# Kernel tuning notes

Measured on AMD Instinct MI355X. Metric: run time of the kernel, lower is better.

Reference implementation:

```python
import jax, jax.numpy as jnp
import numpy as np

NUM_NODES = 2048
NUM_REL = 8
HIDDEN = 256


def setup_inputs() -> dict:
    key = jax.random.key(0)
    k1, k2, k3 = jax.random.split(key, 3)
    X = jax.random.normal(k1, (NUM_NODES, HIDDEN, NUM_REL), dtype=jnp.float32)
    A = jax.random.uniform(k2, (NUM_NODES, NUM_NODES, NUM_REL), dtype=jnp.float32)
    # nn.init.normal_(std=0.01)
    weight = 0.01 * jax.random.normal(k3, (HIDDEN, HIDDEN, NUM_REL), dtype=jnp.float32)
    return {"X": X, "A": A, "weight": weight}


def _tensor_product(A, B):
    # Faithful to the original: FFT along last (relation) dim, take REAL part of
    # both transformed operands, per-slice matmul, then real part of ifft.
    Af = jnp.real(jnp.fft.fft(A, axis=-1))  # (n1, n2, k)
    Bf = jnp.real(jnp.fft.fft(B, axis=-1))  # (n2, n4, k)
    C = jnp.einsum('nmk,mhk->nhk', Af, Bf)  # batched real matmul over slices k
    return jnp.real(jnp.fft.ifft(C, axis=-1)).astype(A.dtype)


def reference(X, A, weight):
    res = _tensor_product(A, X)          # (num_nodes, hidden, num_rel)
    res = _tensor_product(res, weight)   # (num_nodes, hidden, num_rel)
    return res
```

## Files before the change

kernel.cpp:

```cpp
#include <hip/hip_runtime.h>


typedef __bf16 bf16_t;
typedef __bf16 bf16x2 __attribute__((ext_vector_type(2)));
typedef __bf16 bf16x8 __attribute__((ext_vector_type(8)));
typedef float f32x4 __attribute__((ext_vector_type(4)));

#define R2C 0.70710678118654752f

__device__ __forceinline__ size_t swz(int r, int c, int K) {
  return (size_t)r * K + (c & ~63) + ((((c >> 3) & 7) ^ (r & 7)) << 3) + (c & 7);
}

__device__ __forceinline__ void async_cp16(const void* g, void* l) {
  __builtin_amdgcn_global_load_lds((const __attribute__((address_space(1))) char*)g,
                                   (__attribute__((address_space(3))) char*)l,
                                   16, 0, 0);
}

__device__ __forceinline__ void fwd5(const float x[8], float F[5]) {
  float s04 = x[0] + x[4], d04 = x[0] - x[4];
  float s26 = x[2] + x[6];
  float s15 = x[1] + x[5], s37 = x[3] + x[7];
  float t = (x[1] + x[7]) - (x[3] + x[5]);
  float e = s04 + s26, o = s15 + s37;
  F[0] = e + o;
  F[1] = d04 + R2C * t;
  F[2] = s04 - s26;
  F[3] = d04 - R2C * t;
  F[4] = e - o;
}

__global__ __launch_bounds__(256) void k_pre(const float* __restrict__ X,
                                             const float* __restrict__ A,
                                             const float* __restrict__ W,
                                             bf16_t* __restrict__ Xft,
                                             bf16_t* __restrict__ Af,
                                             bf16_t* __restrict__ Wft) {
  __shared__ bf16_t tx[40][256];
  int b = blockIdx.x;
  if (b < 2048) {
    size_t t = (size_t)b * 256 + threadIdx.x;
    size_t idx = t * 8;
    int n = (int)(idx >> 11), m8 = (int)(idx & 2047);
    const f32x4* p = (const f32x4*)(A + idx * 8);
    float F[8][5];
#pragma unroll
    for (int u = 0; u < 8; u++) {
      f32x4 a = __builtin_nontemporal_load(p + 2 * u);
      f32x4 bb = __builtin_nontemporal_load(p + 2 * u + 1);
      float x[8] = {a.x, a.y, a.z, a.w, bb.x, bb.y, bb.z, bb.w};
      fwd5(x, F[u]);
    }
    size_t pos = (size_t)n * 2048 + (m8 & ~63) + ((((m8 >> 3) & 7) ^ (n & 7)) << 3);
#pragma unroll
    for (int j = 0; j < 5; j++) {
      bf16x8 v = {(bf16_t)F[0][j], (bf16_t)F[1][j], (bf16_t)F[2][j],
                  (bf16_t)F[3][j], (bf16_t)F[4][j], (bf16_t)F[5][j],
                  (bf16_t)F[6][j], (bf16_t)F[7][j]};
      *(bf16x8*)(Af + (size_t)j * 4194304 + pos) = v;
    }
  } else if (b < 2304) {
    int bx = b - 2048;
    int m0 = (bx & 7) * 256, h0 = (bx >> 3) * 8;
    int t = threadIdx.x;
    const float4* p = (const float4*)(X + (((size_t)(m0 + t) * 256) + h0) * 8);
#pragma unroll
    for (int h = 0; h < 8; h++) {
      float4 a = p[2 * h], bb = p[2 * h + 1];
      float x[8] = {a.x, a.y, a.z, a.w, bb.x, bb.y, bb.z, bb.w};
      float F[5];
      fwd5(x, F);
#pragma unroll
      for (int j = 0; j < 5; j++) tx[j * 8 + h][t] = (bf16_t)F[j];
    }
    __syncthreads();
#pragma unroll
    for (int it = 0; it < 5; it++) {
      int slot = it * 256 + t;
      int row = slot >> 5, ch = slot & 31;
      int j = row >> 3, hl = row & 7;
      int h = h0 + hl;
      size_t gpos = (size_t)j * 524288 + (size_t)h * 2048 + m0 +
                    ((ch & ~7) << 3) + (((ch & 7) ^ (h & 7)) << 3);
      *(uint4*)(Xft + gpos) = *(const uint4*)(&tx[row][ch * 8]);
    }
  } else {
    int h = b - 2304;
    int hp = threadIdx.x;
    const float4* p = (const float4*)(W + ((size_t)hp * 256 + h) * 8);
    float4 a = p[0], bb = p[1];
    float x[8] = {a.x, a.y, a.z, a.w, bb.x, bb.y, bb.z, bb.w};
    float F[5];
    fwd5(x, F);
    const float sc[5] = {0.125f, 0.25f, 0.25f, 0.25f, 0.125f};
    size_t pos = swz(h, hp, 256);
#pragma unroll
    for (int j = 0; j < 5; j++)
      Wft[(size_t)j * 65536 + pos] = (bf16_t)(F[j] * sc[j]);
  }
}

template <typename OutT, bool SWZ_OUT, int BH>
__global__ __launch_bounds__(256) void gemm_lds(const bf16_t* __restrict__ A,
                                                const bf16_t* __restrict__ B,
                                                OutT* __restrict__ C, int K,
                                                size_t ap, size_t bp, size_t cp) {
  constexpr int WH = BH / 2;
  constexpr int NT = WH / 16;
  constexpr int BR = BH / 32;
  constexpr int ABUF = 128 * 64;
  constexpr int BBUF = BH * 64;
  __shared__ bf16_t sm[2 * ABUF + 2 * BBUF];
  const int j = blockIdx.z;
  const bf16_t* Aj = A + (size_t)j * ap;
  const bf16_t* Bj = B + (size_t)j * bp;
  OutT* Cj = C + (size_t)j * cp;
  const int n0 = blockIdx.x * 128, h0 = blockIdx.y * BH;
  const int tid = threadIdx.x;
  const int wv = tid >> 6, ln = tid & 63;
  const int quad = ln >> 4, l16 = ln & 15;
  const int wn = (wv & 1) * 64, wh = (wv >> 1) * WH;

  const bf16_t* ga[4];
  int loA[4];
#pragma unroll
  for (int s = 0; s < 4; s++) {
    int slot = s * 256 + tid;
    int row = slot >> 3, c16 = slot & 7;
    ga[s] = Aj + (size_t)(n0 + row) * K + c16 * 8;
    loA[s] = (s * 256 + wv * 64) * 8;
  }
  const bf16_t* gb[BR];
  int loB[BR];
#pragma unroll
  for (int s = 0; s < BR; s++) {
    int slot = s * 256 + tid;
    int row = slot >> 3, c16 = slot & 7;
    gb[s] = Bj + (size_t)(h0 + row) * K + c16 * 8;
    loB[s] = (s * 256 + wv * 64) * 8;
  }

#pragma unroll
  for (int s = 0; s < 4; s++) async_cp16(ga[s], sm + loA[s]);
#pragma unroll
  for (int s = 0; s < BR; s++) async_cp16(gb[s], sm + 2 * ABUF + loB[s]);

  f32x4 acc[4][NT] = {};
  for (int kk = 0; kk < K; kk += 64) {
    int p = (kk >> 6) & 1;
    if (kk + 64 < K) {
#pragma unroll
      for (int s = 0; s < 4; s++)
        async_cp16(ga[s] + kk + 64, sm + (p ^ 1) * ABUF + loA[s]);
#pragma unroll
      for (int s = 0; s < BR; s++)
        async_cp16(gb[s] + kk + 64, sm + 2 * ABUF + (p ^ 1) * BBUF + loB[s]);
      __builtin_amdgcn_s_waitcnt(0xF70 | (4 + BR));
    } else {
      __builtin_amdgcn_s_waitcnt(0xF70);
    }
    __builtin_amdgcn_s_barrier();
    const bf16_t* Asp = sm + p * ABUF;
    const bf16_t* Bsp = sm + 2 * ABUF + p * BBUF;
#pragma unroll
    for (int kh = 0; kh < 2; kh++) {
      bf16x8 af[4], bfr[NT];
      int c16 = kh * 4 + quad;
#pragma unroll
      for (int i = 0; i < 4; i++) {
        int ra = wn + i * 16 + l16;
        af[i] = *(const bf16x8*)(Asp + ra * 64 + ((c16 ^ (ra & 7)) << 3));
      }
#pragma unroll
      for (int t = 0; t < NT; t++) {
        int rb = wh + t * 16 + l16;
        bfr[t] = *(const bf16x8*)(Bsp + rb * 64 + ((c16 ^ (rb & 7)) << 3));
      }
#pragma unroll
      for (int i = 0; i < 4; i++)
#pragma unroll
        for (int t = 0; t < NT; t++)
          acc[i][t] = __builtin_amdgcn_mfma_f32_16x16x32_bf16(af[i], bfr[t],
                                                              acc[i][t], 0, 0, 0);
    }
    __builtin_amdgcn_s_barrier();
  }
#pragma unroll
  for (int i = 0; i < 4; i++) {
#pragma unroll
    for (int t = 0; t < NT; t++) {
      int hc = h0 + wh + t * 16 + l16;
#pragma unroll
      for (int rg = 0; rg < 4; rg++) {
        int nr = n0 + wn + i * 16 + quad * 4 + rg;
        size_t off = SWZ_OUT ? swz(nr, hc, 256) : (size_t)nr * 256 + hc;
        Cj[off] = (OutT)acc[i][t][rg];
      }
    }
  }
}

__global__ __launch_bounds__(256) void k_combine(const float* __restrict__ C2,
                                                 float* __restrict__ out) {
  size_t idx = (size_t)blockIdx.x * 256 + threadIdx.x;
  float c0 = C2[idx];
  float c1 = C2[524288 + idx];
  float c2 = C2[2 * 524288 + idx];
  float c3 = C2[3 * 524288 + idx];
  float c4 = C2[4 * 524288 + idx];
  float o0 = c0 + c1 + c2 + c3 + c4;
  float o4 = c0 - c1 + c2 - c3 + c4;
  float o2 = c0 - c2 + c4;
  float rt = R2C * (c1 - c3);
  float o1 = c0 + rt - c4;
  float o3 = c0 - rt - c4;
  float4* op = (float4*)(out + idx * 8);
  op[0] = make_float4(o0, o1, o2, o3);
  op[1] = make_float4(o4, o3, o2, o1);
}

extern "C" void kernel_launch(void* const* d_in, const int* in_sizes, int n_in,
                              void* d_out, int out_size, void* d_ws, size_t ws_size,
                              hipStream_t stream) {
  const float* X = (const float*)d_in[0];
  const float* A = (const float*)d_in[1];
  const float* W = (const float*)d_in[2];
  float* out = (float*)d_out;
  char* ws = (char*)d_ws;

  bf16_t* Af  = (bf16_t*)(ws);
  bf16_t* Xft = (bf16_t*)(ws + 41943040);
  bf16_t* Wft = (bf16_t*)(ws + 47185920);
  bf16_t* C1  = (bf16_t*)(ws + 47841280);
  float*  C2  = (float*) (ws + 53084160);

  k_pre<<<dim3(2560), 256, 0, stream>>>(X, A, W, Xft, Af, Wft);
  gemm_lds<bf16_t, true, 64><<<dim3(16, 4, 5), 256, 0, stream>>>(
      Af, Xft, C1, 2048, (size_t)4194304, (size_t)524288, (size_t)524288);
  gemm_lds<float, false, 128><<<dim3(16, 2, 5), 256, 0, stream>>>(
      C1, Wft, C2, 256, (size_t)524288, (size_t)65536, (size_t)524288);
  k_combine<<<dim3(2048), 256, 0, stream>>>(C2, out);
}
```

Measured before the change: 277.6 us.

## Stage A-row FFT through LDS for coalesced loads; widen first GEMM tile

The A preprocessing now assigns one block per node row. Each block loads the row in coalesced float4 chunks, transposes the data through shared memory so every thread handles one column's 8 relations, and writes the bf16 FFT outputs with 16-byte swizzled stores. This replaces the previous path where each thread read a strided 256-byte span of A. The first GEMM also moves from 64-wide to 128-wide H tiles, which halves the grid and increases reuse of the A fragments. The cost is extra barriers per row, more LDS use, and a first GEMM with only 160 blocks, which may underfill the GPU.

```diff
diff --git a/kernel.cpp b/kernel.cpp
--- a/kernel.cpp
+++ b/kernel.cpp
@@ -37,33 +37,52 @@
                                              bf16_t* __restrict__ Xft,
                                              bf16_t* __restrict__ Af,
                                              bf16_t* __restrict__ Wft) {
-  __shared__ bf16_t tx[40][256];
+  __shared__ __align__(16) char sm_raw[28672];
   int b = blockIdx.x;
+  int t = threadIdx.x;
   if (b < 2048) {
-    size_t t = (size_t)b * 256 + threadIdx.x;
-    size_t idx = t * 8;
-    int n = (int)(idx >> 11), m8 = (int)(idx & 2047);
-    const f32x4* p = (const f32x4*)(A + idx * 8);
-    float F[8][5];
-#pragma unroll
-    for (int u = 0; u < 8; u++) {
-      f32x4 a = __builtin_nontemporal_load(p + 2 * u);
-      f32x4 bb = __builtin_nontemporal_load(p + 2 * u + 1);
-      float x[8] = {a.x, a.y, a.z, a.w, bb.x, bb.y, bb.z, bb.w};
-      fwd5(x, F[u]);
-    }
-    size_t pos = (size_t)n * 2048 + (m8 & ~63) + ((((m8 >> 3) & 7) ^ (n & 7)) << 3);
+    float* st = (float*)sm_raw;
+    bf16_t* ob = (bf16_t*)(sm_raw + 8192);
+    const int n = b;
+    const f32x4* Arow = (const f32x4*)(A + (size_t)n * 16384);
+#pragma unroll 1
+    for (int r = 0; r < 8; r++) {
+      f32x4 q0 = Arow[r * 512 + t];
+      f32x4 q1 = Arow[r * 512 + 256 + t];
+      __syncthreads();
+      {
+        int e0 = t >> 1, h0 = (t & 1) * 4;
+        st[(h0 + 0) * 256 + e0] = q0.x;
+        st[(h0 + 1) * 256 + e0] = q0.y;
+        st[(h0 + 2) * 256 + e0] = q0.z;
+        st[(h0 + 3) * 256 + e0] = q0.w;
+        int e1 = e0 + 128;
+        st[(h0 + 0) * 256 + e1] = q1.x;
+        st[(h0 + 1) * 256 + e1] = q1.y;
+        st[(h0 + 2) * 256 + e1] = q1.z;
+        st[(h0 + 3) * 256 + e1] = q1.w;
+      }
+      __syncthreads();
+      float x[8];
+#pragma unroll
+      for (int k = 0; k < 8; k++) x[k] = st[k * 256 + t];
+      float F[5];
+      fwd5(x, F);
+#pragma unroll
+      for (int j = 0; j < 5; j++) ob[j * 2048 + r * 256 + t] = (bf16_t)F[j];
+    }
+    __syncthreads();
 #pragma unroll
     for (int j = 0; j < 5; j++) {
-      bf16x8 v = {(bf16_t)F[0][j], (bf16_t)F[1][j], (bf16_t)F[2][j],
-                  (bf16_t)F[3][j], (bf16_t)F[4][j], (bf16_t)F[5][j],
-                  (bf16_t)F[6][j], (bf16_t)F[7][j]};
-      *(bf16x8*)(Af + (size_t)j * 4194304 + pos) = v;
+      uint4 v = *(const uint4*)(ob + j * 2048 + t * 8);
+      size_t gpos = (size_t)j * 4194304 + (size_t)n * 2048 + ((t * 8) & ~63) +
+                    (((t & 7) ^ (n & 7)) << 3);
+      *(uint4*)(Af + gpos) = v;
     }
   } else if (b < 2304) {
+    bf16_t* tx = (bf16_t*)sm_raw;
     int bx = b - 2048;
     int m0 = (bx & 7) * 256, h0 = (bx >> 3) * 8;
-    int t = threadIdx.x;
     const float4* p = (const float4*)(X + (((size_t)(m0 + t) * 256) + h0) * 8);
 #pragma unroll
     for (int h = 0; h < 8; h++) {
@@ -72,7 +91,7 @@
       float F[5];
       fwd5(x, F);
 #pragma unroll
-      for (int j = 0; j < 5; j++) tx[j * 8 + h][t] = (bf16_t)F[j];
+      for (int j = 0; j < 5; j++) tx[(j * 8 + h) * 256 + t] = (bf16_t)F[j];
     }
     __syncthreads();
 #pragma unroll
@@ -83,11 +102,11 @@
       int h = h0 + hl;
       size_t gpos = (size_t)j * 524288 + (size_t)h * 2048 + m0 +
                     ((ch & ~7) << 3) + (((ch & 7) ^ (h & 7)) << 3);
-      *(uint4*)(Xft + gpos) = *(const uint4*)(&tx[row][ch * 8]);
+      *(uint4*)(Xft + gpos) = *(const uint4*)(&tx[row * 256 + ch * 8]);
     }
   } else {
     int h = b - 2304;
-    int hp = threadIdx.x;
+    int hp = t;
     const float4* p = (const float4*)(W + ((size_t)hp * 256 + h) * 8);
     float4 a = p[0], bb = p[1];
     float x[8] = {a.x, a.y, a.z, a.w, bb.x, bb.y, bb.z, bb.w};
@@ -236,7 +255,7 @@
   float*  C2  = (float*) (ws + 53084160);
 
   k_pre<<<dim3(2560), 256, 0, stream>>>(X, A, W, Xft, Af, Wft);
-  gemm_lds<bf16_t, true, 64><<<dim3(16, 4, 5), 256, 0, stream>>>(
+  gemm_lds<bf16_t, true, 128><<<dim3(16, 2, 5), 256, 0, stream>>>(
       Af, Xft, C1, 2048, (size_t)4194304, (size_t)524288, (size_t)524288);
   gemm_lds<float, false, 128><<<dim3(16, 2, 5), 256, 0, stream>>>(
       C1, Wft, C2, 256, (size_t)524288, (size_t)65536, (size_t)524288);
```

Result: faster. 258.4 us (-6.9%).
